# Performance work log

Hardware: AMD Instinct MI355X
Metric: run time of the kernel (lower is better)

The kernel has to match this reference:

```python
import jax, jax.numpy as jnp
import numpy as np

B, N, A = 8, 8192, 10   # batch, points, attributes (xyz + normal + 4 extra)
G, M = 512, 32          # num_group, group_size
EPS = 1e-5


def setup_inputs() -> dict:
    key = jax.random.key(0)
    ks = jax.random.split(key, 16)
    w = lambda k, s: jax.random.normal(k, s, jnp.float32) * 0.02
    inp = {"xyz": jax.random.normal(ks[0], (B, N, A), jnp.float32)}
    # Light_T_Net params (conv1 6->64, conv2 64->512, fc 512->36)
    inp["tn_w1"], inp["tn_b1"] = w(ks[1], (64, 6)), jnp.zeros(64, jnp.float32)
    inp["tn_g1"], inp["tn_be1"] = jnp.ones(64, jnp.float32), jnp.zeros(64, jnp.float32)
    inp["tn_w2"], inp["tn_b2"] = w(ks[2], (512, 64)), jnp.zeros(512, jnp.float32)
    inp["tn_g2"], inp["tn_be2"] = jnp.ones(512, jnp.float32), jnp.zeros(512, jnp.float32)
    inp["tn_fw"], inp["tn_fb"] = w(ks[3], (36, 512)), jnp.zeros(36, jnp.float32)
    # Light_PointNet_Encoder convs: A->128->256->512->1024
    for i, (co, ci) in enumerate([(128, A), (256, 128), (512, 256), (1024, 512)], 1):
        inp[f"w{i}"], inp[f"b{i}"] = w(ks[3 + i], (co, ci)), jnp.zeros(co, jnp.float32)
        inp[f"g{i}"], inp[f"be{i}"] = jnp.ones(co, jnp.float32), jnp.zeros(co, jnp.float32)
    return inp


def _bn(x, g, b):
    # training-mode BatchNorm1d: stats over (batch, length) for [BG, n, C]
    m = x.mean((0, 1))
    v = x.var((0, 1))
    return (x - m) * jax.lax.rsqrt(v + EPS) * g + b


def _fps(xyz, npoint):
    # sequential farthest-point sampling (deterministic start index 0)
    coords = xyz[:, :, :3]
    b, n, _ = xyz.shape

    def step(carry, _):
        dist, far = carry
        cen = jnp.take_along_axis(xyz, far[:, None, None], axis=1)  # [B,1,A]
        d = jnp.sum((coords - cen[:, :, :3]) ** 2, -1)              # [B,N]
        dist = jnp.minimum(dist, d)
        return (dist, jnp.argmax(dist, -1)), (far, cen[:, 0, :])

    dist0 = jnp.full((b, n), 1e10, xyz.dtype)
    far0 = jnp.zeros((b,), jnp.int32)
    _, (idx, attrs) = jax.lax.scan(step, (dist0, far0), None, length=npoint)
    return idx.T, attrs.transpose(1, 0, 2)  # [B,G], [B,G,A]


def _forward(xyz, tn_w1, tn_b1, tn_g1, tn_be1, tn_w2, tn_b2, tn_g2, tn_be2,
             tn_fw, tn_fb, w1, b1, g1, be1, w2, b2, g2, be2,
             w3, b3, g3, be3, w4, b4, g4, be4):
    b = xyz.shape[0]
    # ---- Group_for_all_attribute ----
    _, cen = _fps(xyz, G)                                           # [B,G,A]
    # cdist over full attribute dim; squared distance gives identical topk order
    d2 = (jnp.sum(cen ** 2, -1)[:, :, None] + jnp.sum(xyz ** 2, -1)[:, None, :]
          - 2.0 * jnp.einsum('bga,bna->bgn', cen, xyz))             # [B,G,N]
    idx = jax.lax.top_k(-d2, M)[1]                                  # [B,G,M] smallest dists
    nb = xyz[jnp.arange(b)[:, None, None], idx]                     # [B,G,M,A]
    nb = jnp.concatenate([nb[..., :3] - cen[:, :, None, :3], nb[..., 3:]], -1)
    # ---- Light_PointNet_Encoder ----
    pg = nb.reshape(b * G, M, A)
    x6 = pg[:, :, :6]
    # Light_T_Net
    h = jax.nn.relu(_bn(x6 @ tn_w1.T + tn_b1, tn_g1, tn_be1))
    h = jax.nn.relu(_bn(h @ tn_w2.T + tn_b2, tn_g2, tn_be2))
    t = (h.max(1) @ tn_fw.T + tn_fb + jnp.eye(6, dtype=xyz.dtype).reshape(36)).reshape(-1, 6, 6)
    pg = jnp.concatenate([jnp.einsum('bnc,bcd->bnd', x6, t), pg[:, :, 6:]], -1)
    # 1x1 conv stack (= per-point linear) with training-mode BN
    h = jax.nn.relu(_bn(pg @ w1.T + b1, g1, be1))
    h = jax.nn.relu(_bn(h @ w2.T + b2, g2, be2))
    h = jax.nn.relu(_bn(h @ w3.T + b3, g3, be3))
    h = _bn(h @ w4.T + b4, g4, be4)
    return h.max(1).reshape(b, G, -1)                               # [B,G,1024]


def reference(xyz, tn_w1, tn_b1, tn_g1, tn_be1, tn_w2, tn_b2, tn_g2, tn_be2,
              tn_fw, tn_fb, w1, b1, g1, be1, w2, b2, g2, be2,
              w3, b3, g3, be3, w4, b4, g4, be4):
    return _forward(xyz, tn_w1, tn_b1, tn_g1, tn_be1, tn_w2, tn_b2, tn_g2, tn_be2,
                    tn_fw, tn_fb, w1, b1, g1, be1, w2, b2, g2, be2,
                    w3, b3, g3, be3, w4, b4, g4, be4)
```

## Files before the change

### kernel.cpp

```cpp
#include <hip/hip_runtime.h>
#include <hip/hip_bf16.h>

static constexpr int B_  = 8;
static constexpr int N_  = 8192;
static constexpr int A_  = 10;
static constexpr int G_  = 512;
static constexpr int M_  = 32;
static constexpr int S_TOT = B_ * G_ * M_;
static constexpr float EPS_ = 1e-5f;
static constexpr float FMAXV = 3.402823466e+38f;

__device__ __forceinline__ float b2f(__hip_bfloat16 h) { return __bfloat162float(h); }
__device__ __forceinline__ unsigned short f2bs(float f) {
    __hip_bfloat16 h = __float2bfloat16(f);
    return *reinterpret_cast<unsigned short*>(&h);
}

typedef __bf16 bf16x8 __attribute__((ext_vector_type(8)));
typedef float  f32x4  __attribute__((ext_vector_type(4)));

__device__ __forceinline__ unsigned long long shfl_down_u64(unsigned long long v, int off) {
    unsigned lo = (unsigned)v, hi = (unsigned)(v >> 32);
    lo = __shfl_down(lo, off);
    hi = __shfl_down(hi, off);
    return ((unsigned long long)hi << 32) | lo;
}

static constexpr size_t CO_XYZ  = 0;
static constexpr size_t CO_TNW1 = 655360, CO_TNB1 = 655744, CO_TNG1 = 655808, CO_TNBE1 = 655872;
static constexpr size_t CO_TNW2 = 655936, CO_TNB2 = 688704, CO_TNG2 = 689216, CO_TNBE2 = 689728;
static constexpr size_t CO_TNFW = 690240, CO_TNFB = 708672;
static constexpr size_t CO_W1 = 708708, CO_B1 = 709988, CO_G1 = 710116, CO_BE1 = 710244;
static constexpr size_t CO_W2 = 710372, CO_B2 = 743140, CO_G2 = 743396, CO_BE2 = 743652;
static constexpr size_t CO_W3 = 743908, CO_B3 = 874980, CO_G3 = 875492, CO_BE3 = 876004;
static constexpr size_t CO_W4 = 876516, CO_B4 = 1400804, CO_G4 = 1401828, CO_BE4 = 1402852;
static constexpr size_t CO_TOT = 1403876;

static constexpr size_t WB_TNW2 = 0;
static constexpr size_t WB_W2   = 32768;
static constexpr size_t WB_W3   = 65536;
static constexpr size_t WB_W4   = 196608;
static constexpr size_t WB_TOT  = 720896;

#define MB_ (1024ull * 1024ull)
static constexpr size_t OFF_CANON = 0;
static constexpr size_t OFF_CEN   = 6 * MB_;
static constexpr size_t OFF_XSQ   = 6 * MB_ + 256 * 1024;
static constexpr size_t OFF_STATS = 6 * MB_ + 512 * 1024;
static constexpr size_t OFF_COEFF = 6 * MB_ + 576 * 1024;
static constexpr size_t OFF_DUMMY = 6 * MB_ + 640 * 1024;
static constexpr size_t OFF_TMAT  = 6 * MB_ + 768 * 1024;
static constexpr size_t OFF_WBF16 = 8 * MB_;
static constexpr size_t OFF_PG    = 10 * MB_;
static constexpr size_t OFF_TZ1   = 16 * MB_;
static constexpr size_t OFF_TPMAX = 32 * MB_;
static constexpr size_t OFF_TPMIN = 40 * MB_;
static constexpr size_t OFF_Z1    = 16 * MB_;
static constexpr size_t OFF_MM4X  = 16 * MB_;
static constexpr size_t OFF_MM4N  = 32 * MB_;
static constexpr size_t OFF_Z2    = 48 * MB_;
static constexpr size_t OFF_Z3    = 112 * MB_;
static constexpr size_t NEED_A = 240 * MB_;
static constexpr int NCHUNK_ = 8;
static constexpr int CSAMP_  = S_TOT / NCHUNK_;

static constexpr int STF_T1 = 0;
static constexpr int STF_T2 = 128;
static constexpr int STF_M1 = 1152;
static constexpr int STF_M2 = 1408;
static constexpr int STF_M3 = 1920;
static constexpr int STF_M4 = 2944;

struct Ptrs { const void* p[27]; };

__global__ __launch_bounds__(256)
void zero_kernel(float* __restrict__ p, int n)
{
    for (int i = threadIdx.x; i < n; i += 256) p[i] = 0.f;
}

__global__ __launch_bounds__(256)
void convert_kernel(Ptrs ptrs, float* __restrict__ canon)
{
    const size_t gid = (size_t)blockIdx.x * 256 + threadIdx.x;
    if (gid >= CO_TOT) return;
    constexpr size_t offs[28] = {0, 655360, 655744, 655808, 655872, 655936,
        688704, 689216, 689728, 690240, 708672, 708708, 709988, 710116, 710244,
        710372, 743140, 743396, 743652, 743908, 874980, 875492, 876004, 876516,
        1400804, 1401828, 1402852, 1403876};
    int j = 0;
    while (j < 26 && gid >= offs[j + 1]) ++j;
    const size_t loc = gid - offs[j];
    const bool fp32m = (((const unsigned short*)ptrs.p[3])[0] == 0);
    float v;
    if (fp32m) v = ((const float*)ptrs.p[j])[loc];
    else       v = b2f(((const __hip_bfloat16*)ptrs.p[j])[loc]);
    canon[gid] = v;
}

__global__ __launch_bounds__(256)
void wconv_kernel(const float* __restrict__ canon, __hip_bfloat16* __restrict__ wb)
{
    const size_t gid = (size_t)blockIdx.x * 256 + threadIdx.x;
    if (gid >= WB_TOT) return;
    constexpr size_t offs[5] = {0, 32768, 65536, 196608, 720896};
    constexpr size_t co[4]   = {CO_TNW2, CO_W2, CO_W3, CO_W4};
    int j = 0;
    while (j < 3 && gid >= offs[j + 1]) ++j;
    wb[gid] = __float2bfloat16(canon[co[j] + (gid - offs[j])]);
}

__global__ __launch_bounds__(512)
void fps_kernel(const float* __restrict__ xyz, float* __restrict__ cen)
{
    __shared__ unsigned long long red[2][8];
    __shared__ int fidx[G_];

    const int t = threadIdx.x;
    const int b = blockIdx.x;
    const float* xb = xyz + (size_t)b * N_ * A_;

    float px[16], py[16], pz[16], dist[16];
#pragma unroll
    for (int j = 0; j < 16; ++j) {
        const int i = j * 512 + t;
        px[j] = xb[(size_t)i * A_ + 0];
        py[j] = xb[(size_t)i * A_ + 1];
        pz[j] = xb[(size_t)i * A_ + 2];
        dist[j] = 1e10f;
    }
    __syncthreads();

    int far = 0;
    for (int it = 0; it < G_; ++it) {
        if (t == 0) fidx[it] = far;
        const float2 cxy = *reinterpret_cast<const float2*>(xb + (size_t)far * A_);
        const float  cz  = xb[(size_t)far * A_ + 2];

        unsigned long long best = 0;
#pragma unroll
        for (int j = 0; j < 16; ++j) {
            const float dx = px[j] - cxy.x, dy = py[j] - cxy.y, dz = pz[j] - cz;
            const float d = dx * dx + dy * dy + dz * dz;
            const float nd = fminf(dist[j], d);
            dist[j] = nd;
            const unsigned long long pk =
                ((unsigned long long)__float_as_uint(nd) << 32) |
                (unsigned)~(unsigned)(j * 512 + t);
            best = (pk > best) ? pk : best;
        }
#pragma unroll
        for (int off = 32; off; off >>= 1) {
            const unsigned long long o = shfl_down_u64(best, off);
            best = (o > best) ? o : best;
        }
        if ((t & 63) == 0) red[it & 1][t >> 6] = best;
        __syncthreads();
        unsigned long long m = red[it & 1][0];
#pragma unroll
        for (int w = 1; w < 8; ++w) {
            const unsigned long long o = red[it & 1][w];
            m = (o > m) ? o : m;
        }
        far = (int)(~(unsigned)m);
    }
    __syncthreads();
    for (int e = t; e < G_ * A_; e += 512) {
        const int it = e / A_;
        const int a  = e - it * A_;
        cen[((size_t)b * G_ + it) * A_ + a] = xb[(size_t)fidx[it] * A_ + a];
    }
}

__global__ __launch_bounds__(256)
void xsq_kernel(const float* __restrict__ xyz, float* __restrict__ xsq)
{
    const int i = blockIdx.x * 256 + threadIdx.x;
    float s = 0.f;
#pragma unroll
    for (int a = 0; a < A_; ++a) { const float v = xyz[(size_t)i * A_ + a]; s += v * v; }
    xsq[i] = s;
}

__global__ __launch_bounds__(256)
void knn_kernel(const float* __restrict__ xyz, const float* __restrict__ cen,
                const float* __restrict__ xsq, float* __restrict__ pg)
{
    __shared__ float d2[N_];
    __shared__ float ca[A_];
    __shared__ float csqs;
    __shared__ float redV[4];
    __shared__ int   redI[4];
    __shared__ int   win[M_];
    __shared__ int   curwin;

    const int t  = threadIdx.x;
    const int bg = blockIdx.x;
    const int b  = bg >> 9;
    const float* xb  = xyz + (size_t)b * N_ * A_;
    const float* xsb = xsq + (size_t)b * N_;

    if (t < A_) ca[t] = cen[(size_t)bg * A_ + t];
    __syncthreads();
    if (t == 0) {
        float s = 0.f;
        for (int a = 0; a < A_; ++a) s += ca[a] * ca[a];
        csqs = s;
    }
    __syncthreads();
    const float csq = csqs;

    for (int j = 0; j < 32; ++j) {
        const int i = j * 256 + t;
        float dot = 0.f;
#pragma unroll
        for (int a = 0; a < A_; ++a) dot += xb[(size_t)i * A_ + a] * ca[a];
        d2[i] = (csq + xsb[i]) - 2.f * dot;
    }
    __syncthreads();

    float bv = FMAXV; int bi = 0;
    for (int j = 0; j < 32; ++j) {
        const int i = j * 256 + t;
        const float v = d2[i];
        if (v < bv) { bv = v; bi = i; }
    }

    for (int it = 0; it < M_; ++it) {
        float rv = bv; int ri = bi;
#pragma unroll
        for (int off = 32; off; off >>= 1) {
            const float ov = __shfl_down(rv, off);
            const int   oi = __shfl_down(ri, off);
            if (ov < rv || (ov == rv && oi < ri)) { rv = ov; ri = oi; }
        }
        if ((t & 63) == 0) { redV[t >> 6] = rv; redI[t >> 6] = ri; }
        __syncthreads();
        if (t == 0) {
            float v = redV[0]; int wi = redI[0];
            for (int w = 1; w < 4; ++w)
                if (redV[w] < v || (redV[w] == v && redI[w] < wi)) { v = redV[w]; wi = redI[w]; }
            win[it] = wi; curwin = wi; d2[wi] = FMAXV;
        }
        __syncthreads();
        const int wi = curwin;
        if ((wi & 255) == t) {
            bv = FMAXV; bi = 0;
            for (int j = 0; j < 32; ++j) {
                const int i = j * 256 + t;
                const float v = d2[i];
                if (v < bv) { bv = v; bi = i; }
            }
        }
    }
    __syncthreads();
    if (t < M_) {
        const int i = win[t];
        for (int a = 0; a < A_; ++a) {
            float v = xb[(size_t)i * A_ + a];
            if (a < 3) v -= ca[a];
            pg[((size_t)bg * M_ + t) * A_ + a] = v;
        }
    }
}

template<int K, int C>
__global__ __launch_bounds__(256)
void mlp_small_kernel(const float* __restrict__ pgx,
                      const float* __restrict__ W,
                      const float* __restrict__ Bv,
                      __hip_bfloat16* __restrict__ Zout,
                      float* __restrict__ stats)
{
    __shared__ float w[C * K];
    __shared__ float bb[C];
    __shared__ float lstat[C][2];
    const int t = threadIdx.x;
    for (int i = t; i < C * K; i += 256) w[i] = W[i];
    for (int i = t; i < C; i += 256) bb[i] = Bv[i];
    for (int i = t; i < 2 * C; i += 256) ((float*)lstat)[i] = 0.f;
    __syncthreads();

    const size_t s = (size_t)blockIdx.x * 256 + t;
    float x[K];
#pragma unroll
    for (int k = 0; k < K; ++k) x[k] = pgx[s * A_ + k];

    ushort4 u;
    for (int c = 0; c < C; ++c) {
        float z = bb[c];
#pragma unroll
        for (int k = 0; k < K; ++k) z += w[c * K + k] * x[k];
        const unsigned short zs = f2bs(z);
        const int cm = c & 3;
        if (cm == 0) u.x = zs; else if (cm == 1) u.y = zs; else if (cm == 2) u.z = zs;
        else { u.w = zs; *reinterpret_cast<ushort4*>(Zout + s * C + (c - 3)) = u; }

        float sv = z, sq = z * z;
#pragma unroll
        for (int off = 32; off; off >>= 1) {
            sv += __shfl_down(sv, off);
            sq += __shfl_down(sq, off);
        }
        if ((t & 63) == 0) { atomicAdd(&lstat[c][0], sv); atomicAdd(&lstat[c][1], sq); }
    }
    __syncthreads();
    for (int c = t; c < C; c += 256) {
        atomicAdd(&stats[c],     lstat[c][0]);
        atomicAdd(&stats[C + c], lstat[c][1]);
    }
}

__global__ __launch_bounds__(256)
void finalize_kernel(const float* __restrict__ stats, const float* __restrict__ g,
                     const float* __restrict__ be, float* __restrict__ coeff, int C)
{
    for (int c = threadIdx.x; c < C; c += 256) {
        const float mean = stats[c] * (1.f / (float)S_TOT);
        const float var  = stats[C + c] * (1.f / (float)S_TOT) - mean * mean;
        const float sc = g[c] * rsqrtf(fmaxf(var, 0.f) + EPS_);
        coeff[c]     = sc;
        coeff[C + c] = be[c] - mean * sc;
    }
}

template<int K, int N, bool POOL>
__global__ __launch_bounds__(256)
void gemm_mfma_kernel(const __hip_bfloat16* __restrict__ Zin,
                      const float* __restrict__ coeff,
                      const __hip_bfloat16* __restrict__ Wb,
                      const float* __restrict__ Bv,
                      __hip_bfloat16* __restrict__ Zout,
                      float* __restrict__ maxbuf,
                      float* __restrict__ minbuf,
                      float* __restrict__ stats)
{
    constexpr int PITCH = 72;
    __shared__ __hip_bfloat16 As[128 * PITCH];
    __shared__ __hip_bfloat16 Bs[128 * PITCH];
    __shared__ float csc[K];
    __shared__ float csh[K];
    __shared__ float lstat[256];

    const int t    = threadIdx.x;
    const int lane = t & 63;
    const int wave = t >> 6;
    const int wm   = wave >> 1;
    const int wn   = wave & 1;
    const int ln   = lane & 15;
    const int quad = lane >> 4;
    const int c0   = blockIdx.x * 128;
    const int s0   = blockIdx.y * 128;

    for (int i = t; i < K; i += 256) { csc[i] = coeff[i]; csh[i] = coeff[K + i]; }
    lstat[t] = 0.f;

    f32x4 acc[4][4];
#pragma unroll
    for (int ni = 0; ni < 4; ++ni) {
        const float bj = Bv[c0 + wn * 64 + ni * 16 + ln];
#pragma unroll
        for (int mi = 0; mi < 4; ++mi) acc[mi][ni] = (f32x4){bj, bj, bj, bj};
    }

    for (int kt = 0; kt < K; kt += 64) {
        __syncthreads();
#pragma unroll
        for (int p = 0; p < 4; ++p) {
            const int id = p * 256 + t;
            const int r  = id >> 3;
            const int sg = id & 7;
            const float4 raw = *reinterpret_cast<const float4*>(
                Zin + (size_t)(s0 + r) * K + kt + sg * 8);
            const __hip_bfloat162* p2 = reinterpret_cast<const __hip_bfloat162*>(&raw);
            unsigned short tmp[8] __attribute__((aligned(16)));
#pragma unroll
            for (int j = 0; j < 4; ++j) {
                const int k0 = kt + sg * 8 + 2 * j;
                const float x0 = fmaxf(b2f(p2[j].x) * csc[k0]     + csh[k0],     0.f);
                const float x1 = fmaxf(b2f(p2[j].y) * csc[k0 + 1] + csh[k0 + 1], 0.f);
                tmp[2 * j]     = f2bs(x0);
                tmp[2 * j + 1] = f2bs(x1);
            }
            *reinterpret_cast<float4*>(&As[r * PITCH + sg * 8]) =
                *reinterpret_cast<const float4*>(tmp);
            *reinterpret_cast<float4*>(&Bs[r * PITCH + sg * 8]) =
                *reinterpret_cast<const float4*>(Wb + (size_t)(c0 + r) * K + kt + sg * 8);
        }
        __syncthreads();

        bf16x8 af[4][2], bf_[4][2];
#pragma unroll
        for (int mi = 0; mi < 4; ++mi)
#pragma unroll
            for (int kk = 0; kk < 2; ++kk)
                af[mi][kk] = *reinterpret_cast<const bf16x8*>(
                    &As[(wm * 64 + mi * 16 + ln) * PITCH + quad * 8 + kk * 32]);
#pragma unroll
        for (int ni = 0; ni < 4; ++ni)
#pragma unroll
            for (int kk = 0; kk < 2; ++kk)
                bf_[ni][kk] = *reinterpret_cast<const bf16x8*>(
                    &Bs[(wn * 64 + ni * 16 + ln) * PITCH + quad * 8 + kk * 32]);
#pragma unroll
        for (int kk = 0; kk < 2; ++kk)
#pragma unroll
            for (int mi = 0; mi < 4; ++mi)
#pragma unroll
                for (int ni = 0; ni < 4; ++ni)
                    acc[mi][ni] = __builtin_amdgcn_mfma_f32_16x16x32_bf16(
                        af[mi][kk], bf_[ni][kk], acc[mi][ni], 0, 0, 0);
    }

#pragma unroll
    for (int ni = 0; ni < 4; ++ni) {
        float sv = 0.f, sq = 0.f;
#pragma unroll
        for (int mi = 0; mi < 4; ++mi)
#pragma unroll
            for (int r = 0; r < 4; ++r) {
                const float v = acc[mi][ni][r];
                sv += v; sq += v * v;
            }
        sv += __shfl_xor(sv, 16); sq += __shfl_xor(sq, 16);
        sv += __shfl_xor(sv, 32); sq += __shfl_xor(sq, 32);
        if (quad == 0) {
            const int col = wn * 64 + ni * 16 + ln;
            atomicAdd(&lstat[col], sv);
            atomicAdd(&lstat[128 + col], sq);
        }
    }
    __syncthreads();
    if (t < 128) {
        atomicAdd(&stats[c0 + t],     lstat[t]);
        atomicAdd(&stats[N + c0 + t], lstat[128 + t]);
    }

    if constexpr (POOL) {
#pragma unroll
        for (int ni = 0; ni < 4; ++ni) {
            float mx0 = -FMAXV, mn0 = FMAXV, mx1 = -FMAXV, mn1 = FMAXV;
#pragma unroll
            for (int mi = 0; mi < 2; ++mi)
#pragma unroll
                for (int r = 0; r < 4; ++r) {
                    const float v = acc[mi][ni][r];
                    mx0 = fmaxf(mx0, v); mn0 = fminf(mn0, v);
                }
#pragma unroll
            for (int mi = 2; mi < 4; ++mi)
#pragma unroll
                for (int r = 0; r < 4; ++r) {
                    const float v = acc[mi][ni][r];
                    mx1 = fmaxf(mx1, v); mn1 = fminf(mn1, v);
                }
            mx0 = fmaxf(mx0, __shfl_xor(mx0, 16)); mn0 = fminf(mn0, __shfl_xor(mn0, 16));
            mx0 = fmaxf(mx0, __shfl_xor(mx0, 32)); mn0 = fminf(mn0, __shfl_xor(mn0, 32));
            mx1 = fmaxf(mx1, __shfl_xor(mx1, 16)); mn1 = fminf(mn1, __shfl_xor(mn1, 16));
            mx1 = fmaxf(mx1, __shfl_xor(mx1, 32)); mn1 = fminf(mn1, __shfl_xor(mn1, 32));
            if (quad == 0) {
                const int col = c0 + wn * 64 + ni * 16 + ln;
                const int g   = (s0 >> 5) + wm * 2;
                maxbuf[(size_t)g * N + col]       = mx0;
                minbuf[(size_t)g * N + col]       = mn0;
                maxbuf[(size_t)(g + 1) * N + col] = mx1;
                minbuf[(size_t)(g + 1) * N + col] = mn1;
            }
        }
    } else {
#pragma unroll
        for (int mi = 0; mi < 4; ++mi)
#pragma unroll
            for (int r = 0; r < 4; ++r) {
                const size_t row = (size_t)(s0 + wm * 64 + mi * 16 + quad * 4 + r);
#pragma unroll
                for (int ni = 0; ni < 4; ++ni) {
                    const int col = c0 + wn * 64 + ni * 16 + ln;
                    Zout[row * N + col] = __float2bfloat16(acc[mi][ni][r]);
                }
            }
    }
}

__global__ __launch_bounds__(64)
void tnet_fc_kernel(const float* __restrict__ maxbuf, const float* __restrict__ minbuf,
                    const float* __restrict__ coeff, const float* __restrict__ FW,
                    const float* __restrict__ FB, float* __restrict__ tmat)
{
    __shared__ float h[512];
    const int bg = blockIdx.x;
    const int t  = threadIdx.x;
    for (int i = t; i < 512; i += 64) {
        const float sc = coeff[i], sh = coeff[512 + i];
        const float v = (sc >= 0.f) ? maxbuf[(size_t)bg * 512 + i] : minbuf[(size_t)bg * 512 + i];
        h[i] = fmaxf(sc * v + sh, 0.f);
    }
    __syncthreads();
    if (t < 36) {
        float acc = FB[t] + ((t % 7 == 0) ? 1.f : 0.f);
        for (int k = 0; k < 512; ++k) acc += FW[t * 512 + k] * h[k];
        tmat[(size_t)bg * 36 + t] = acc;
    }
}

__global__ __launch_bounds__(256)
void transform_kernel(float* __restrict__ pg, const float* __restrict__ tmat)
{
    const size_t s = (size_t)blockIdx.x * 256 + threadIdx.x;
    const int bg = (int)(s >> 5);
    float x[6];
#pragma unroll
    for (int c = 0; c < 6; ++c) x[c] = pg[s * A_ + c];
    const float* tm = tmat + (size_t)bg * 36;
#pragma unroll
    for (int d = 0; d < 6; ++d) {
        float o = 0.f;
#pragma unroll
        for (int c = 0; c < 6; ++c) o += x[c] * tm[c * 6 + d];
        pg[s * A_ + d] = o;
    }
}

__global__ __launch_bounds__(256)
void output_kernel(const float* __restrict__ maxbuf, const float* __restrict__ minbuf,
                   const float* __restrict__ coeff, const unsigned short* __restrict__ probe,
                   void* __restrict__ out)
{
    const size_t e = (size_t)blockIdx.x * 256 + threadIdx.x;
    const int c = (int)(e & 1023);
    const float sc = coeff[c], sh = coeff[1024 + c];
    const float v = (sc >= 0.f) ? maxbuf[e] : minbuf[e];
    const float r = sc * v + sh;
    if (probe[0] == 0) ((float*)out)[e] = r;
    else ((__hip_bfloat16*)out)[e] = __float2bfloat16(r);
}

extern "C" void kernel_launch(void* const* d_in, const int* in_sizes, int n_in,
                              void* d_out, int out_size, void* d_ws, size_t ws_size,
                              hipStream_t stream)
{
    char* ws = (char*)d_ws;
    float*          canon = (float*)(ws + OFF_CANON);
    float*          cen   = (float*)(ws + OFF_CEN);
    float*          xsq   = (float*)(ws + OFF_XSQ);
    float*          stats = (float*)(ws + OFF_STATS);
    float*          coeff = (float*)(ws + OFF_COEFF);
    float*          dummy = (float*)(ws + OFF_DUMMY);
    float*          tmat  = (float*)(ws + OFF_TMAT);
    __hip_bfloat16* wbf   = (__hip_bfloat16*)(ws + OFF_WBF16);
    float*          tpmax = (float*)(ws + OFF_TPMAX);
    float*          tpmin = (float*)(ws + OFF_TPMIN);
    float*          pg    = (float*)(ws + OFF_PG);
    __hip_bfloat16* tz1   = (__hip_bfloat16*)(ws + OFF_TZ1);
    __hip_bfloat16* z1    = (__hip_bfloat16*)(ws + OFF_Z1);
    __hip_bfloat16* z2    = (__hip_bfloat16*)(ws + OFF_Z2);
    __hip_bfloat16* z3    = (__hip_bfloat16*)(ws + OFF_Z3);
    float*          mmax4 = (float*)(ws + OFF_MM4X);
    float*          mmin4 = (float*)(ws + OFF_MM4N);

    Ptrs ptrs;
    for (int i = 0; i < 27; ++i) ptrs.p[i] = d_in[i];

    const float* cxyz = canon + CO_XYZ;

    zero_kernel<<<1, 256, 0, stream>>>(stats, 5120);
    convert_kernel<<<(int)((CO_TOT + 255) / 256), 256, 0, stream>>>(ptrs, canon);
    wconv_kernel<<<(int)((WB_TOT + 255) / 256), 256, 0, stream>>>(canon, wbf);

    fps_kernel<<<B_, 512, 0, stream>>>(cxyz, cen);
    xsq_kernel<<<(B_ * N_) / 256, 256, 0, stream>>>(cxyz, xsq);
    knn_kernel<<<B_ * G_, 256, 0, stream>>>(cxyz, cen, xsq, pg);

    mlp_small_kernel<6, 64><<<S_TOT / 256, 256, 0, stream>>>(
        pg, canon + CO_TNW1, canon + CO_TNB1, tz1, stats + STF_T1);
    finalize_kernel<<<1, 256, 0, stream>>>(stats + STF_T1, canon + CO_TNG1, canon + CO_TNBE1,
                                           coeff + STF_T1, 64);
    gemm_mfma_kernel<64, 512, true><<<dim3(4, S_TOT / 128), 256, 0, stream>>>(
        tz1, coeff + STF_T1, wbf + WB_TNW2, canon + CO_TNB2, nullptr, tpmax, tpmin, stats + STF_T2);
    finalize_kernel<<<1, 256, 0, stream>>>(stats + STF_T2, canon + CO_TNG2, canon + CO_TNBE2,
                                           coeff + STF_T2, 512);
    tnet_fc_kernel<<<B_ * G_, 64, 0, stream>>>(tpmax, tpmin, coeff + STF_T2,
                                               canon + CO_TNFW, canon + CO_TNFB, tmat);
    transform_kernel<<<S_TOT / 256, 256, 0, stream>>>(pg, tmat);

    mlp_small_kernel<10, 128><<<S_TOT / 256, 256, 0, stream>>>(
        pg, canon + CO_W1, canon + CO_B1, z1, stats + STF_M1);
    finalize_kernel<<<1, 256, 0, stream>>>(stats + STF_M1, canon + CO_G1, canon + CO_BE1,
                                           coeff + STF_M1, 128);
    gemm_mfma_kernel<128, 256, false><<<dim3(2, S_TOT / 128), 256, 0, stream>>>(
        z1, coeff + STF_M1, wbf + WB_W2, canon + CO_B2, z2, nullptr, nullptr, stats + STF_M2);
    finalize_kernel<<<1, 256, 0, stream>>>(stats + STF_M2, canon + CO_G2, canon + CO_BE2,
                                           coeff + STF_M2, 256);

    if (ws_size >= NEED_A) {
        gemm_mfma_kernel<256, 512, false><<<dim3(4, S_TOT / 128), 256, 0, stream>>>(
            z2, coeff + STF_M2, wbf + WB_W3, canon + CO_B3, z3, nullptr, nullptr, stats + STF_M3);
        finalize_kernel<<<1, 256, 0, stream>>>(stats + STF_M3, canon + CO_G3, canon + CO_BE3,
                                               coeff + STF_M3, 512);
        gemm_mfma_kernel<512, 1024, true><<<dim3(8, S_TOT / 128), 256, 0, stream>>>(
            z3, coeff + STF_M3, wbf + WB_W4, canon + CO_B4, nullptr, mmax4, mmin4, stats + STF_M4);
    } else {
        for (int c = 0; c < NCHUNK_; ++c) {
            gemm_mfma_kernel<256, 512, false><<<dim3(4, CSAMP_ / 128), 256, 0, stream>>>(
                z2 + (size_t)c * CSAMP_ * 256, coeff + STF_M2, wbf + WB_W3, canon + CO_B3,
                z3, nullptr, nullptr, stats + STF_M3);
        }
        finalize_kernel<<<1, 256, 0, stream>>>(stats + STF_M3, canon + CO_G3, canon + CO_BE3,
                                               coeff + STF_M3, 512);
        for (int c = 0; c < NCHUNK_; ++c) {
            gemm_mfma_kernel<256, 512, false><<<dim3(4, CSAMP_ / 128), 256, 0, stream>>>(
                z2 + (size_t)c * CSAMP_ * 256, coeff + STF_M2, wbf + WB_W3, canon + CO_B3,
                z3, nullptr, nullptr, dummy);
            gemm_mfma_kernel<512, 1024, true><<<dim3(8, CSAMP_ / 128), 256, 0, stream>>>(
                z3, coeff + STF_M3, wbf + WB_W4, canon + CO_B4, nullptr,
                mmax4 + (size_t)(c * CSAMP_ / 32) * 1024,
                mmin4 + (size_t)(c * CSAMP_ / 32) * 1024, stats + STF_M4);
        }
    }
    finalize_kernel<<<1, 256, 0, stream>>>(stats + STF_M4, canon + CO_G4, canon + CO_BE4,
                                           coeff + STF_M4, 1024);

    output_kernel<<<(B_ * G_ * 1024) / 256, 256, 0, stream>>>(
        mmax4, mmin4, coeff + STF_M4, (const unsigned short*)d_in[3], d_out);
}
```

Baseline: 1.600 ms.

## Replace FPS barrier with tag spin-wait and split BN stats into separate kernel

In the farthest-point-sampling kernel, the per-iteration __syncthreads is replaced by per-wave flags in shared memory that each thread spins on, to cut barrier cost across the 512 serial iterations. Separately, the per-channel wave-shuffle reductions and LDS atomics in the small MLP kernels are removed. Batch-norm statistics are now computed by a new stats kernel that re-reads the bf16 outputs. This trades extra memory reads and launches for less shuffle work, and the stats now come from bf16-rounded values rather than fp32. The spin-wait relies on intra-block memory ordering and may risk livelock or ordering bugs.

Result: slower. 1.949 ms (+21.8%).

```diff
diff --git a/kernel.cpp b/kernel.cpp
--- a/kernel.cpp
+++ b/kernel.cpp
@@ -114,6 +114,7 @@
 void fps_kernel(const float* __restrict__ xyz, float* __restrict__ cen)
 {
     __shared__ unsigned long long red[2][8];
+    __shared__ int tags[2][8];
     __shared__ int fidx[G_];
 
     const int t = threadIdx.x;
@@ -129,6 +130,7 @@
         pz[j] = xb[(size_t)i * A_ + 2];
         dist[j] = 1e10f;
     }
+    if (t < 16) tags[t >> 3][t & 7] = 0;
     __syncthreads();
 
     int far = 0;
@@ -154,12 +156,26 @@
             const unsigned long long o = shfl_down_u64(best, off);
             best = (o > best) ? o : best;
         }
-        if ((t & 63) == 0) red[it & 1][t >> 6] = best;
-        __syncthreads();
-        unsigned long long m = red[it & 1][0];
+        const int p = it & 1;
+        if ((t & 63) == 0) {
+            red[p][t >> 6] = best;
+            __threadfence_block();
+            *(volatile int*)&tags[p][t >> 6] = it + 1;
+        }
+        {
+            volatile int* tg = &tags[p][0];
+            bool ready;
+            do {
+                ready = true;
+#pragma unroll
+                for (int w = 0; w < 8; ++w) ready = ready && (tg[w] >= it + 1);
+            } while (!ready);
+        }
+        volatile unsigned long long* rd = &red[p][0];
+        unsigned long long m = rd[0];
 #pragma unroll
         for (int w = 1; w < 8; ++w) {
-            const unsigned long long o = red[it & 1][w];
+            const unsigned long long o = rd[w];
             m = (o > m) ? o : m;
         }
         far = (int)(~(unsigned)m);
@@ -269,16 +285,13 @@
 void mlp_small_kernel(const float* __restrict__ pgx,
                       const float* __restrict__ W,
                       const float* __restrict__ Bv,
-                      __hip_bfloat16* __restrict__ Zout,
-                      float* __restrict__ stats)
+                      __hip_bfloat16* __restrict__ Zout)
 {
     __shared__ float w[C * K];
     __shared__ float bb[C];
-    __shared__ float lstat[C][2];
     const int t = threadIdx.x;
     for (int i = t; i < C * K; i += 256) w[i] = W[i];
     for (int i = t; i < C; i += 256) bb[i] = Bv[i];
-    for (int i = t; i < 2 * C; i += 256) ((float*)lstat)[i] = 0.f;
     __syncthreads();
 
     const size_t s = (size_t)blockIdx.x * 256 + t;
@@ -287,6 +300,7 @@
     for (int k = 0; k < K; ++k) x[k] = pgx[s * A_ + k];
 
     ushort4 u;
+#pragma unroll 4
     for (int c = 0; c < C; ++c) {
         float z = bb[c];
 #pragma unroll
@@ -295,19 +309,33 @@
         const int cm = c & 3;
         if (cm == 0) u.x = zs; else if (cm == 1) u.y = zs; else if (cm == 2) u.z = zs;
         else { u.w = zs; *reinterpret_cast<ushort4*>(Zout + s * C + (c - 3)) = u; }
-
-        float sv = z, sq = z * z;
-#pragma unroll
-        for (int off = 32; off; off >>= 1) {
-            sv += __shfl_down(sv, off);
-            sq += __shfl_down(sq, off);
-        }
-        if ((t & 63) == 0) { atomicAdd(&lstat[c][0], sv); atomicAdd(&lstat[c][1], sq); }
-    }
-    __syncthreads();
-    for (int c = t; c < C; c += 256) {
-        atomicAdd(&stats[c],     lstat[c][0]);
-        atomicAdd(&stats[C + c], lstat[c][1]);
+    }
+}
+
+template<int C>
+__global__ __launch_bounds__(256)
+void stats_kernel(const __hip_bfloat16* __restrict__ Z, float* __restrict__ stats)
+{
+    __shared__ float ls[2 * C];
+    constexpr int L = 256 / C;
+    const int t   = threadIdx.x;
+    const int c   = t & (C - 1);
+    const int sub = t / C;
+    for (int i = t; i < 2 * C; i += 256) ls[i] = 0.f;
+    __syncthreads();
+
+    float sv = 0.f, sq = 0.f;
+    const size_t s0 = (size_t)blockIdx.x * 1024;
+    for (int k = 0; k < 1024 / L; ++k) {
+        const float v = b2f(Z[(s0 + sub + (size_t)k * L) * C + c]);
+        sv += v; sq += v * v;
+    }
+    atomicAdd(&ls[c], sv);
+    atomicAdd(&ls[C + c], sq);
+    __syncthreads();
+    for (int i = t; i < C; i += 256) {
+        atomicAdd(&stats[i],     ls[i]);
+        atomicAdd(&stats[C + i], ls[C + i]);
     }
 }
 
@@ -572,7 +600,8 @@
     knn_kernel<<<B_ * G_, 256, 0, stream>>>(cxyz, cen, xsq, pg);
 
     mlp_small_kernel<6, 64><<<S_TOT / 256, 256, 0, stream>>>(
-        pg, canon + CO_TNW1, canon + CO_TNB1, tz1, stats + STF_T1);
+        pg, canon + CO_TNW1, canon + CO_TNB1, tz1);
+    stats_kernel<64><<<S_TOT / 1024, 256, 0, stream>>>(tz1, stats + STF_T1);
     finalize_kernel<<<1, 256, 0, stream>>>(stats + STF_T1, canon + CO_TNG1, canon + CO_TNBE1,
                                            coeff + STF_T1, 64);
     gemm_mfma_kernel<64, 512, true><<<dim3(4, S_TOT / 128), 256, 0, stream>>>(
@@ -584,7 +613,8 @@
     transform_kernel<<<S_TOT / 256, 256, 0, stream>>>(pg, tmat);
 
     mlp_small_kernel<10, 128><<<S_TOT / 256, 256, 0, stream>>>(
-        pg, canon + CO_W1, canon + CO_B1, z1, stats + STF_M1);
+        pg, canon + CO_W1, canon + CO_B1, z1);
+    stats_kernel<128><<<S_TOT / 1024, 256, 0, stream>>>(z1, stats + STF_M1);
     finalize_kernel<<<1, 256, 0, stream>>>(stats + STF_M1, canon + CO_G1, canon + CO_BE1,
                                            coeff + STF_M1, 128);
     gemm_mfma_kernel<128, 256, false><<<dim3(2, S_TOT / 128), 256, 0, stream>>>(
```
